# Kernel tuning notes

Measured on AMD Instinct MI355X. Metric: run time of the kernel, lower is better.

## Reference

```python
import jax, jax.numpy as jnp
import numpy as np

EPS = 1e-5

def _bn(x, s, b, m, v):
    # inference-mode BatchNorm2d over channel axis of NCHW
    return (x - m[None, :, None, None]) * jax.lax.rsqrt(v[None, :, None, None] + EPS) \
           * s[None, :, None, None] + b[None, :, None, None]

def _conv3(x, w):
    return jax.lax.conv_general_dilated(x, w, (1, 1), 'SAME',
                                        dimension_numbers=('NCHW', 'OIHW', 'NCHW'))

def _conv1(x, w, b):
    # 1x1 conv as einsum; w: [out_c, in_c]
    return jnp.einsum('oc,bchw->bohw', w, x) + b[None, :, None, None]

def _cca(f, qw, qb, kw, kb, vw, vb, gamma):
    # Criss-cross attention (faithful to source: no diagonal -inf masking, INF() unused there)
    B, C, H, W = f.shape
    q = _conv1(f, qw, qb)   # [B, C/8, H, W]
    k = _conv1(f, kw, kb)   # [B, C/8, H, W]
    v = _conv1(f, vw, vb)   # [B, C,   H, W]
    # energy along column (same w, all h') and row (same h, all w')
    eH = jnp.einsum('bchw,bciw->bhwi', q, k)            # [B,H,W,H]
    eW = jnp.einsum('bchw,bchj->bhwj', q, k)            # [B,H,W,W]
    att = jax.nn.softmax(jnp.concatenate([eH, eW], axis=3), axis=3)  # [B,H,W,H+W]
    aH, aW = att[..., :H], att[..., H:]
    oH = jnp.einsum('bhwi,bciw->bchw', aH, v)
    oW = jnp.einsum('bhwj,bchj->bchw', aW, v)
    return gamma * (oH + oW) + f


def setup_inputs() -> dict:
    key = jax.random.key(0)
    ks = iter(jax.random.split(key, 64))
    B, Cin, H, W = 8, 2048, 64, 64
    Ci, Cq, Co = 256, 32, 512
    rn = lambda s, sc=0.02: jax.random.normal(next(ks), s, jnp.float32) * sc
    ru = lambda s: jax.random.uniform(next(ks), s, jnp.float32)
    return {
        'x': jax.random.normal(next(ks), (B, Cin, H, W), jnp.float32),
        'recurrence': 2,
        'conva_w': rn((Ci, Cin, 3, 3)),
        'bn_a_s': ru((Ci,)), 'bn_a_b': rn((Ci,), 0.1), 'bn_a_m': rn((Ci,), 0.1), 'bn_a_v': ru((Ci,)),
        'q_w': rn((Cq, Ci)), 'q_b': rn((Cq,), 0.1),
        'k_w': rn((Cq, Ci)), 'k_b': rn((Cq,), 0.1),
        'v_w': rn((Ci, Ci)), 'v_b': rn((Ci,), 0.1),
        'cca_gamma': rn((1,), 1.0),
        'convb_w': rn((Ci, Ci, 3, 3)),
        'bn_b_s': ru((Ci,)), 'bn_b_b': rn((Ci,), 0.1), 'bn_b_m': rn((Ci,), 0.1), 'bn_b_v': ru((Ci,)),
        'sq_w': rn((Ci, Ci)), 'sq_b': rn((Ci,), 0.1),
        'bn_g_s': ru((Ci,)), 'bn_g_b': rn((Ci,), 0.1), 'bn_g_m': rn((Ci,), 0.1), 'bn_g_v': ru((Ci,)),
        'fc1_w': rn((Ci // 2, Ci)), 'fc1_b': rn((Ci // 2,), 0.1),
        'fc2_w': rn((Ci, Ci // 2)), 'fc2_b': rn((Ci,), 0.1),
        'bott_w': rn((Co, Cin + 2 * Ci, 3, 3)),
        'bn_t_s': ru((Co,)), 'bn_t_b': rn((Co,), 0.1), 'bn_t_m': rn((Co,), 0.1), 'bn_t_v': ru((Co,)),
    }


def reference(x, recurrence, conva_w, bn_a_s, bn_a_b, bn_a_m, bn_a_v,
              q_w, q_b, k_w, k_b, v_w, v_b, cca_gamma,
              convb_w, bn_b_s, bn_b_b, bn_b_m, bn_b_v,
              sq_w, sq_b, bn_g_s, bn_g_b, bn_g_m, bn_g_v,
              fc1_w, fc1_b, fc2_w, fc2_b,
              bott_w, bn_t_s, bn_t_b, bn_t_m, bn_t_v):
    out = _bn(_conv3(x, conva_w), bn_a_s, bn_a_b, bn_a_m, bn_a_v)
    # Global_Avg_Pooling (SE gating) on conva output
    fm = jax.nn.relu(_bn(_conv1(out, sq_w, sq_b), bn_g_s, bn_g_b, bn_g_m, bn_g_v))
    vec = fm.mean(axis=(-2, -1))                       # [B, Ci]
    h = jax.nn.relu(vec @ fc1_w.T + fc1_b)
    gate = jax.nn.sigmoid(h @ fc2_w.T + fc2_b)
    out_gap = out * gate[:, :, None, None]
    # recurrent criss-cross attention
    for _ in range(recurrence):
        out = _cca(out, q_w, q_b, k_w, k_b, v_w, v_b, cca_gamma)
    out = _bn(_conv3(out, convb_w), bn_b_s, bn_b_b, bn_b_m, bn_b_v)
    cat = jnp.concatenate([x, out, out_gap], axis=1)   # [B, Cin+2*Ci, H, W]
    return _bn(_conv3(cat, bott_w), bn_t_s, bn_t_b, bn_t_m, bn_t_v)
```

## Files before the change

kernel.cpp:

```cpp
#include <hip/hip_runtime.h>
#include <hip/hip_bf16.h>

typedef unsigned short u16;
typedef unsigned int u32;
typedef __attribute__((ext_vector_type(8))) short short8;
typedef __attribute__((ext_vector_type(8))) unsigned short u16x8;
typedef __attribute__((ext_vector_type(4))) unsigned short u16x4;
typedef __attribute__((ext_vector_type(4))) float f32x4;

#define BN_EPS 1e-5f
#define PADW 66
#define CATC 2560

__device__ __forceinline__ u16 f2b(float f) {
    __hip_bfloat16 h = __float2bfloat16(f);
    return *reinterpret_cast<u16*>(&h);
}
__device__ __forceinline__ float b2f(u16 u) {
    __hip_bfloat16 h;
    *reinterpret_cast<u16*>(&h) = u;
    return __bfloat162float(h);
}
__device__ __forceinline__ void async_copy16(void* lds, const void* g) {
    __builtin_amdgcn_global_load_lds((const __attribute__((address_space(1))) u32*)g,
                                     (__attribute__((address_space(3))) u32*)lds, 16, 0, 0);
}
__device__ __forceinline__ void fence_() { asm volatile("" ::: "memory"); }
__device__ __forceinline__ void barrier_() { fence_(); __builtin_amdgcn_s_barrier(); fence_(); }

template<int TAPS, int BN, int EPI, int CPT, int NTILES, int KSPLIT>
__global__ __launch_bounds__(512, 2)
void gemm8(const u16* __restrict__ Ag, int cstride,
           const u16* __restrict__ Bg, int ktot_full, int klen,
           const float* __restrict__ alpha, const float* __restrict__ beta,
           u16* __restrict__ outb, int ostride, int ochoff,
           float* __restrict__ outf, int nch)
{
    constexpr int WN   = BN / 4;
    constexpr int NSUB = WN / 16;
    constexpr int NQ   = NSUB / 2;
    constexpr int BLH  = BN / 128;
    constexpr int ASZ  = 256 * 128;
    constexpr int BSZ  = BN * 128;
    const int KT = klen / 64;

    extern __shared__ __align__(16) char smem[];
    char* smA = smem;
    char* smB = smem + 2 * ASZ;

    const int tid  = threadIdx.x;
    const int lane = tid & 63;
    const int wave = tid >> 6;
    const int wr = wave >> 2;
    const int wc = wave & 3;

    const int nwg = gridDim.x;
    const int wg  = blockIdx.x;
    const int swz = (wg & 7) * (nwg >> 3) + (wg >> 3);
    const int sel = swz % (NTILES * KSPLIT);
    const int m0  = (swz / (NTILES * KSPLIT)) * 256;
    const int n0  = (sel / KSPLIT) * BN;
    const int ks  = sel % KSPLIT;
    const int kstart = ks * klen;

    const int sr = tid >> 3;
    const int sc = tid & 7;
    const int scx8 = (sc ^ (sr & 7)) * 8;
    long baseAe[4];
#pragma unroll
    for (int j = 0; j < 4; ++j) {
        int p = m0 + j * 64 + sr;
        int b = p >> 12, h = (p >> 6) & 63, w = p & 63;
        long apix = (TAPS == 1) ? ((long)(b * PADW + h + 1) * PADW + (w + 1))
                                : ((long)(b * PADW + h) * PADW + w);
        baseAe[j] = apix * cstride + scx8;
    }
    long baseBe[2 * BLH];
#pragma unroll
    for (int h = 0; h < 2; ++h)
#pragma unroll
        for (int l = 0; l < BLH; ++l)
            baseBe[h * BLH + l] = (long)(n0 + h * (BN / 2) + l * 64 + sr) * ktot_full + scx8;

    auto stA = [&](int bsel, int h, long aoff) {
#pragma unroll
        for (int l = 0; l < 2; ++l) {
            const u16* g = Ag + baseAe[2 * h + l] + aoff;
            async_copy16(smA + bsel * ASZ + h * 16384 + l * 8192 + tid * 16, g);
        }
    };
    auto stB = [&](int bsel, int h, int k0) {
#pragma unroll
        for (int l = 0; l < BLH; ++l) {
            const u16* g = Bg + baseBe[h * BLH + l] + k0;
            async_copy16(smB + bsel * BSZ + h * (BSZ / 2) + l * 8192 + tid * 16, g);
        }
    };

    const int rsel  = lane & 15;
    const int cswz0 = (((lane >> 4)     ^ (lane & 7)) << 4);
    const int cswz1 = (((4 | (lane >> 4)) ^ (lane & 7)) << 4);

    f32x4 acc[8][NSUB] = {};
    short8 a[4][2], b0[NQ][2], b1[NQ][2];

    auto ldA = [&](int bsel, int mh) {
        const char* base = smA + bsel * ASZ + (wr * 128 + mh * 64 + rsel) * 128;
#pragma unroll
        for (int mi = 0; mi < 4; ++mi) {
            a[mi][0] = *(const short8*)(base + mi * 2048 + cswz0);
            a[mi][1] = *(const short8*)(base + mi * 2048 + cswz1);
        }
    };
    auto ldB = [&](int bsel, int nh, short8 (&bb)[NQ][2]) {
        const char* base = smB + bsel * BSZ + (wc * WN + nh * (WN / 2) + rsel) * 128;
#pragma unroll
        for (int nj = 0; nj < NQ; ++nj) {
            bb[nj][0] = *(const short8*)(base + nj * 2048 + cswz0);
            bb[nj][1] = *(const short8*)(base + nj * 2048 + cswz1);
        }
    };
    auto quad = [&](int MH, int NH, short8 (&bb)[NQ][2]) {
#pragma unroll
        for (int mi = 0; mi < 4; ++mi)
#pragma unroll
            for (int nj = 0; nj < NQ; ++nj)
#pragma unroll
                for (int kk = 0; kk < 2; ++kk)
                    acc[MH * 4 + mi][NH * NQ + nj] =
                        __builtin_amdgcn_mfma_f32_16x16x32_bf16(
                            a[mi][kk], bb[nj][kk], acc[MH * 4 + mi][NH * NQ + nj], 0, 0, 0);
    };

    const int tap0 = kstart / CPT;
    int c0_ = kstart - tap0 * CPT;
    int dx_ = tap0 % 3;
    long aoff_ = ((long)dx_ + (long)(tap0 / 3) * PADW) * cstride + c0_;
    auto adv = [&]() {
        c0_ += 64; aoff_ += 64;
        if (c0_ == CPT) {
            c0_ = 0; aoff_ += (long)cstride - CPT;
            if (++dx_ == 3) { dx_ = 0; aoff_ += (long)(PADW - 3) * cstride; }
        }
    };

    stA(0, 0, aoff_); stA(0, 1, aoff_); stB(0, 0, kstart); stB(0, 1, kstart);
    adv();
    stB(1, 0, kstart + 64); stB(1, 1, kstart + 64); stA(1, 0, aoff_); stA(1, 1, aoff_);
    long paoff = aoff_;
    adv();
    int skb = kstart + 128;

    if constexpr (BN == 256) asm volatile("s_waitcnt vmcnt(8)" ::: "memory");
    else                     asm volatile("s_waitcnt vmcnt(6)" ::: "memory");
    barrier_();

    for (int kt = 0; kt < KT; ++kt) {
        const int buf = kt & 1;
        ldA(buf, 0); ldB(buf, 0, b0); ldB(buf, 1, b1);
        if (kt >= 1 && kt + 1 < KT) stA(buf ^ 1, 1, paoff);
        barrier_();
        __builtin_amdgcn_s_setprio(1);
        quad(0, 0, b0); quad(0, 1, b1);
        __builtin_amdgcn_s_setprio(0);
        barrier_();
        ldA(buf, 1);
        if (kt + 2 < KT) { stB(buf, 0, skb); stB(buf, 1, skb); stA(buf, 0, aoff_); }
        barrier_();
        __builtin_amdgcn_s_setprio(1);
        quad(1, 0, b0); quad(1, 1, b1);
        __builtin_amdgcn_s_setprio(0);
        if (kt + 2 >= KT) {
            asm volatile("s_waitcnt vmcnt(0)" ::: "memory");
        } else if constexpr (BN == 256) {
            asm volatile("s_waitcnt vmcnt(6)" ::: "memory");
        } else {
            asm volatile("s_waitcnt vmcnt(4)" ::: "memory");
        }
        barrier_();
        paoff = aoff_;
        adv(); skb += 64;
    }

    const int nl = lane & 15, mq = lane >> 4;
#pragma unroll
    for (int s = 0; s < 8; ++s) {
#pragma unroll
        for (int nj = 0; nj < NSUB; ++nj) {
            int n = n0 + wc * WN + nj * 16 + nl;
            float al = (EPI == 4) ? 1.f : alpha[n];
            float be = (EPI == 4) ? 0.f : beta[n];
#pragma unroll
            for (int r = 0; r < 4; ++r) {
                int m = m0 + wr * 128 + s * 16 + mq * 4 + r;
                float v = acc[s][nj][r] * al + be;
                if (EPI == 0) {
                    int b = m >> 12, h = (m >> 6) & 63, w = m & 63;
                    long addr = ((long)(b * PADW + h + 1) * PADW + (w + 1)) * ostride + ochoff + n;
                    outb[addr] = f2b(v);
                } else if (EPI == 2) {
                    int b = m >> 12, h = (m >> 6) & 63, w = m & 63;
                    outf[((long)(b * nch + n) << 12) + (h * 64 + w)] = v;
                } else {
                    outf[(long)ks * ((long)32768 * nch) + (long)m * nch + n] = v;
                }
            }
        }
    }
}

__global__ void combine_k(const float* __restrict__ P,
                          const float* __restrict__ alpha, const float* __restrict__ beta,
                          u16* __restrict__ dst, int dstride, int choff)
{
    int t = threadIdx.x;
    int m = blockIdx.x * 4 + (t >> 6);
    int n = (t & 63) * 4;
    int b = m >> 12, h = (m >> 6) & 63, w = m & 63;
    f32x4 v0 = *(const f32x4*)&P[(long)m * 256 + n];
    f32x4 v1 = *(const f32x4*)&P[(long)32768 * 256 + (long)m * 256 + n];
    f32x4 al = *(const f32x4*)&alpha[n];
    f32x4 be = *(const f32x4*)&beta[n];
    u16x4 r;
#pragma unroll
    for (int i = 0; i < 4; ++i) r[i] = f2b((v0[i] + v1[i]) * al[i] + be[i]);
    *(u16x4*)&dst[((long)(b * PADW + h + 1) * PADW + (w + 1)) * dstride + choff + n] = r;
}

__global__ void border_k(u16* __restrict__ cat, u16* __restrict__ f0)
{
    int i = blockIdx.x;
    int b = i / 260, r = i - b * 260;
    int ph, pw;
    if (r < 66)       { ph = 0;        pw = r; }
    else if (r < 132) { ph = 65;       pw = r - 66; }
    else if (r < 196) { ph = r - 131;  pw = 0; }
    else              { ph = r - 195;  pw = 65; }
    long pix = (long)(b * PADW + ph) * PADW + pw;
    int t = threadIdx.x;
    u16x8 z = {};
    *(u16x8*)&cat[pix * CATC + t * 8] = z;
    if (t < 64) *(u16x8*)&cat[pix * CATC + 2048 + t * 8] = z;
    if (t < 32) *(u16x8*)&f0[pix * 256 + t * 8] = z;
}

template<int TAPS, int EPI>
__global__ __launch_bounds__(256, 2)
void gemm_conv(const u16* __restrict__ A, int cstride, int cpt,
               const u16* __restrict__ Bw, int ktot,
               const float* __restrict__ alpha, const float* __restrict__ beta,
               u16* __restrict__ outb, int ostride, int ochoff,
               float* __restrict__ outf, int n_total)
{
    __shared__ u16 As[128][32];
    __shared__ u16 Bs[128][32];
    __shared__ float red[128];

    const int tid  = threadIdx.x;
    const int lane = tid & 63;
    const int wave = tid >> 6;
    const int wr = wave >> 1, wc = wave & 1;
    const int m0 = blockIdx.y * 128;
    const int n0 = blockIdx.x * 128;

    long pixbase[2];
    long browk[2];
#pragma unroll
    for (int i = 0; i < 2; ++i) {
        int row = i * 64 + (tid >> 2);
        int p = m0 + row;
        int b = p >> 12, h = (p >> 6) & 63, w = p & 63;
        if (TAPS == 1) pixbase[i] = (long)(b * PADW + h + 1) * PADW + (w + 1);
        else           pixbase[i] = (long)(b * PADW + h) * PADW + w;
        browk[i] = (long)(n0 + row) * ktot;
    }
    const int chunk = (tid & 3) * 8;

    f32x4 acc[4][4] = {};

    const int steps = ktot / 32;
    int c0 = 0, dx = 0;
    long toff = 0;
    for (int s = 0; s < steps; ++s) {
        const int k0 = s * 32;
#pragma unroll
        for (int i = 0; i < 2; ++i) {
            const u16* ga = A + (pixbase[i] + ((TAPS == 1) ? 0 : toff)) * cstride + c0 + chunk;
            async_copy16((char*)(&As[0][0]) + i * 4096 + tid * 16, ga);
            const u16* gb = Bw + browk[i] + k0 + chunk;
            async_copy16((char*)(&Bs[0][0]) + i * 4096 + tid * 16, gb);
        }
        asm volatile("s_waitcnt vmcnt(0)" ::: "memory");
        __syncthreads();

        short8 af[4], bf[4];
#pragma unroll
        for (int x = 0; x < 4; ++x) {
            af[x] = *(const short8*)&As[wr * 64 + x * 16 + (lane & 15)][(lane >> 4) * 8];
            bf[x] = *(const short8*)&Bs[wc * 64 + x * 16 + (lane & 15)][(lane >> 4) * 8];
        }
#pragma unroll
        for (int mi = 0; mi < 4; ++mi)
#pragma unroll
            for (int ni = 0; ni < 4; ++ni)
                acc[mi][ni] = __builtin_amdgcn_mfma_f32_16x16x32_bf16(af[mi], bf[ni], acc[mi][ni], 0, 0, 0);
        __syncthreads();

        c0 += 32;
        if (TAPS > 1 && c0 == cpt) {
            c0 = 0; dx++; toff += 1;
            if (dx == 3) { dx = 0; toff += PADW - 3; }
        }
    }

    const int nl = lane & 15;
    const int mq = lane >> 4;

    if (EPI == 3) {
        if (tid < 128) red[tid] = 0.f;
        __syncthreads();
#pragma unroll
        for (int ni = 0; ni < 4; ++ni) {
            int ncol = wc * 64 + ni * 16 + nl;
            int n = n0 + ncol;
            float aa = alpha[n], bb = beta[n];
            float ssum = 0.f;
#pragma unroll
            for (int mi = 0; mi < 4; ++mi)
#pragma unroll
                for (int r = 0; r < 4; ++r)
                    ssum += fmaxf(acc[mi][ni][r] * aa + bb, 0.f);
            atomicAdd(&red[ncol], ssum);
        }
        __syncthreads();
        if (tid < 128) {
            int b = m0 >> 12;
            atomicAdd(&outf[b * 256 + n0 + tid], red[tid]);
        }
    } else {
#pragma unroll
        for (int mi = 0; mi < 4; ++mi) {
#pragma unroll
            for (int r = 0; r < 4; ++r) {
                int m = m0 + wr * 64 + mi * 16 + mq * 4 + r;
#pragma unroll
                for (int ni = 0; ni < 4; ++ni) {
                    int n = n0 + wc * 64 + ni * 16 + nl;
                    float v = acc[mi][ni][r] * alpha[n] + beta[n];
                    outb[(long)m * ostride + n] = f2b(v);
                }
            }
        }
    }
}

__global__ void xpad_k(const float* __restrict__ x, u16* __restrict__ cat)
{
    __shared__ float T[64][68];
    int bh = blockIdx.y;
    int b = bh >> 6, h = bh & 63;
    int c0 = blockIdx.x * 64;
    int t = threadIdx.x;
    const float* xb = x + (((long)b * 2048 + c0) * 64 + h) * 64;
#pragma unroll
    for (int i = 0; i < 4; ++i) {
        int idx = i * 256 + t;
        int c = idx >> 4, wq = (idx & 15) * 4;
        *(f32x4*)&T[c][wq] = *(const f32x4*)&xb[(long)c * 4096 + wq];
    }
    __syncthreads();
    long pbase = ((long)(b * PADW + h + 1) * PADW + 1) * CATC + c0;
#pragma unroll
    for (int j = 0; j < 2; ++j) {
        int idx = j * 256 + t;
        int w = idx >> 3, cg = (idx & 7) * 8;
        u16x8 r;
#pragma unroll
        for (int u = 0; u < 8; ++u) r[u] = f2b(T[cg + u][w]);
        *(u16x8*)&cat[pbase + (long)w * CATC + cg] = r;
    }
}

__global__ void prep_w3(const float* __restrict__ w, u16* __restrict__ o, int O, int C)
{
    int idx = blockIdx.x * 256 + threadIdx.x;
    if (idx >= O * C) return;
    int oo = idx / C, c = idx - oo * C;
    const float* s = w + (long)idx * 9;
    long base = (long)oo * 9 * C + c;
#pragma unroll
    for (int t = 0; t < 9; ++t) o[base + (long)t * C] = f2b(s[t]);
}

__global__ void prep_qkv(const float* __restrict__ qw, const float* __restrict__ kw,
                         const float* __restrict__ vw, u16* __restrict__ o)
{
    int idx = blockIdx.x * 256 + threadIdx.x;
    int n = idx >> 8, c = idx & 255;
    float v;
    if (n < 32) v = qw[n * 256 + c];
    else if (n < 64) v = kw[(n - 32) * 256 + c];
    else if (n < 320) v = vw[(n - 64) * 256 + c];
    else v = 0.f;
    o[idx] = f2b(v);
}

__global__ void prep_cast(const float* __restrict__ w, u16* __restrict__ o, int n)
{
    int i = blockIdx.x * 256 + threadIdx.x;
    if (i < n) o[i] = f2b(w[i]);
}

__global__ void prep_ab(const float* as, const float* ab, const float* am, const float* av,
                        const float* gs, const float* gb, const float* gm, const float* gv, const float* sqb,
                        const float* bs, const float* bb, const float* bm, const float* bv,
                        const float* ts, const float* tb, const float* tm, const float* tv,
                        const float* qb, const float* kb, const float* vb,
                        float* Aa, float* Ba_, float* Ag, float* Bg, float* Ab2, float* Bb2,
                        float* At, float* Bt, float* Aq, float* Bq)
{
    int i = blockIdx.x * 256 + threadIdx.x;
    if (i < 256) { float al = as[i] * rsqrtf(av[i] + BN_EPS); Aa[i] = al; Ba_[i] = ab[i] - am[i] * al; }
    else if (i < 512) { int n = i - 256; float al = gs[n] * rsqrtf(gv[n] + BN_EPS); Ag[n] = al; Bg[n] = gb[n] - gm[n] * al + sqb[n] * al; }
    else if (i < 768) { int n = i - 512; float al = bs[n] * rsqrtf(bv[n] + BN_EPS); Ab2[n] = al; Bb2[n] = bb[n] - bm[n] * al; }
    else if (i < 1280) { int n = i - 768; float al = ts[n] * rsqrtf(tv[n] + BN_EPS); At[n] = al; Bt[n] = tb[n] - tm[n] * al; }
    else if (i < 1664) { int n = i - 1280; Aq[n] = 1.f; Bq[n] = (n < 32) ? qb[n] : (n < 64) ? kb[n - 32] : (n < 320) ? vb[n - 64] : 0.f; }
}

__global__ void gate_k(const float* __restrict__ vacc, const float* __restrict__ fc1w,
                       const float* __restrict__ fc1b, const float* __restrict__ fc2w,
                       const float* __restrict__ fc2b, float* __restrict__ gate)
{
    __shared__ float v[256], hbuf[128];
    int b = blockIdx.x, t = threadIdx.x;
    v[t] = vacc[b * 256 + t] * (1.f / 4096.f);
    __syncthreads();
    if (t < 128) {
        float s = fc1b[t];
        for (int c = 0; c < 256; ++c) s += v[c] * fc1w[t * 256 + c];
        hbuf[t] = fmaxf(s, 0.f);
    }
    __syncthreads();
    float s = fc2b[t];
    for (int j = 0; j < 128; ++j) s += hbuf[j] * fc2w[t * 128 + j];
    gate[b * 256 + t] = 1.f / (1.f + __expf(-s));
}

__global__ void gap_k(const u16* __restrict__ f0, const float* __restrict__ gate, u16* __restrict__ cat)
{
    int p = blockIdx.x, t = threadIdx.x;
    int b = p >> 12, h = (p >> 6) & 63, w = p & 63;
    long ppad = (long)(b * PADW + h + 1) * PADW + (w + 1);
    float f = b2f(f0[ppad * 256 + t]);
    cat[ppad * CATC + 2304 + t] = f2b(f * gate[b * 256 + t]);
}

__global__ void gram_k(const u16* __restrict__ qkv, float* eH, float* eW)
{
    __shared__ u16 Qs[64][32];
    __shared__ u16 Ks[64][32];
    int g = blockIdx.x;
    int mode = g >> 9;
    int bx = g & 511;
    int b = bx >> 6, s = bx & 63;
    float* e = mode ? eW : eH;
    int tid = threadIdx.x, lane = tid & 63, wave = tid >> 6;
    {
        int r = tid >> 2, ch = (tid & 3) * 8;
        long pix = (mode == 0) ? ((long)(b * 64 + r) * 64 + s) : ((long)(b * 64 + s) * 64 + r);
        const u16* gp = qkv + pix * 384;
        *(u16x8*)&Qs[r][ch] = *(const u16x8*)(gp + ch);
        *(u16x8*)&Ks[r][ch] = *(const u16x8*)(gp + 32 + ch);
    }
    __syncthreads();
    f32x4 acc[4] = {};
    short8 a = *(const short8*)&Qs[wave * 16 + (lane & 15)][(lane >> 4) * 8];
#pragma unroll
    for (int ni = 0; ni < 4; ++ni) {
        short8 bb = *(const short8*)&Ks[ni * 16 + (lane & 15)][(lane >> 4) * 8];
        acc[ni] = __builtin_amdgcn_mfma_f32_16x16x32_bf16(a, bb, acc[ni], 0, 0, 0);
    }
#pragma unroll
    for (int ni = 0; ni < 4; ++ni)
#pragma unroll
        for (int r = 0; r < 4; ++r) {
            int row = wave * 16 + (lane >> 4) * 4 + r;
            int col = ni * 16 + (lane & 15);
            long pix = (mode == 0) ? ((long)(b * 64 + row) * 64 + s) : ((long)(b * 64 + s) * 64 + row);
            e[pix * 64 + col] = acc[ni][r];
        }
}

__global__ void softmax_k(const float* __restrict__ eH, const float* __restrict__ eW,
                          u16* __restrict__ aH, u16* __restrict__ aW)
{
    long row = blockIdx.x * 4 + (threadIdx.x >> 6);
    int lane = threadIdx.x & 63;
    float v0 = eH[row * 64 + lane];
    float v1 = eW[row * 64 + lane];
    float m = fmaxf(v0, v1);
#pragma unroll
    for (int off = 32; off; off >>= 1) m = fmaxf(m, __shfl_xor(m, off));
    float e0 = __expf(v0 - m), e1 = __expf(v1 - m);
    float s = e0 + e1;
#pragma unroll
    for (int off = 32; off; off >>= 1) s += __shfl_xor(s, off);
    float inv = 1.f / s;
    aH[row * 64 + lane] = f2b(e0 * inv);
    aW[row * 64 + lane] = f2b(e1 * inv);
}

__global__ __launch_bounds__(256, 2)
void oh_k(const u16* __restrict__ aH, const u16* __restrict__ qkv, float* __restrict__ oHb)
{
    __shared__ float Al[64][68];
    __shared__ u16 Vl[64][264];
    int bx = blockIdx.x;
    int b = bx >> 6, w = bx & 63;
    int t = threadIdx.x;
#pragma unroll
    for (int pass = 0; pass < 2; ++pass) {
        int r = pass * 32 + (t >> 3);
        int ch = (t & 7) * 8;
        u16x8 v = *(const u16x8*)(aH + ((long)(b * 64 + r) * 64 + w) * 64 + ch);
        f32x4 s0, s1;
#pragma unroll
        for (int u = 0; u < 4; ++u) { s0[u] = b2f(v[u]); s1[u] = b2f(v[4 + u]); }
        *(f32x4*)&Al[r][ch] = s0;
        *(f32x4*)&Al[r][ch + 4] = s1;
    }
#pragma unroll
    for (int pass = 0; pass < 8; ++pass) {
        int i = pass * 8 + (t >> 5);
        int ch = (t & 31) * 8;
        *(u16x8*)&Vl[i][ch] = *(const u16x8*)(qkv + ((long)(b * 64 + i) * 64 + w) * 384 + 64 + ch);
    }
    __syncthreads();
    int hb = (t >> 5) * 8, cb = (t & 31) * 8;
    float acc[8][8] = {};
    for (int i = 0; i < 64; ++i) {
        float av[8], vv[8];
        u16x8 v8 = *(const u16x8*)&Vl[i][cb];
#pragma unroll
        for (int u = 0; u < 8; ++u) av[u] = Al[hb + u][i];
#pragma unroll
        for (int u = 0; u < 8; ++u) vv[u] = b2f(v8[u]);
#pragma unroll
        for (int u = 0; u < 8; ++u)
#pragma unroll
            for (int x = 0; x < 8; ++x)
                acc[u][x] += av[u] * vv[x];
    }
#pragma unroll
    for (int u = 0; u < 8; ++u) {
        long base = ((long)(b * 64 + hb + u) * 64 + w) * 256 + cb;
        f32x4 s0, s1;
#pragma unroll
        for (int x = 0; x < 4; ++x) { s0[x] = acc[u][x]; s1[x] = acc[u][4 + x]; }
        *(f32x4*)&oHb[base] = s0;
        *(f32x4*)&oHb[base + 4] = s1;
    }
}

__global__ __launch_bounds__(256, 2)
void ow_k(const u16* __restrict__ aW, const u16* __restrict__ qkv, const float* __restrict__ oHb,
          const u16* __restrict__ fin, u16* __restrict__ fout, const float* __restrict__ gamma_p)
{
    __shared__ float Al[64][68];
    __shared__ u16 Vl[64][264];
    int bx = blockIdx.x;
    int b = bx >> 6, h = bx & 63;
    int t = threadIdx.x;
    float gamma = gamma_p[0];
#pragma unroll
    for (int pass = 0; pass < 2; ++pass) {
        int r = pass * 32 + (t >> 3);
        int ch = (t & 7) * 8;
        u16x8 v = *(const u16x8*)(aW + ((long)(b * 64 + h) * 64 + r) * 64 + ch);
        f32x4 s0, s1;
#pragma unroll
        for (int u = 0; u < 4; ++u) { s0[u] = b2f(v[u]); s1[u] = b2f(v[4 + u]); }
        *(f32x4*)&Al[r][ch] = s0;
        *(f32x4*)&Al[r][ch + 4] = s1;
    }
#pragma unroll
    for (int pass = 0; pass < 8; ++pass) {
        int j = pass * 8 + (t >> 5);
        int ch = (t & 31) * 8;
        *(u16x8*)&Vl[j][ch] = *(const u16x8*)(qkv + ((long)(b * 64 + h) * 64 + j) * 384 + 64 + ch);
    }
    __syncthreads();
    int wb = (t >> 5) * 8, cb = (t & 31) * 8;
    float acc[8][8] = {};
    for (int j = 0; j < 64; ++j) {
        float av[8], vv[8];
        u16x8 v8 = *(const u16x8*)&Vl[j][cb];
#pragma unroll
        for (int u = 0; u < 8; ++u) av[u] = Al[wb + u][j];
#pragma unroll
        for (int u = 0; u < 8; ++u) vv[u] = b2f(v8[u]);
#pragma unroll
        for (int u = 0; u < 8; ++u)
#pragma unroll
            for (int x = 0; x < 8; ++x)
                acc[u][x] += av[u] * vv[x];
    }
#pragma unroll
    for (int u = 0; u < 8; ++u) {
        int w = wb + u;
        long pix = ((long)(b * 64 + h) * 64 + w) * 256 + cb;
        long pp = ((long)(b * PADW + h + 1) * PADW + (w + 1)) * 256 + cb;
        u16x8 f8 = *(const u16x8*)&fin[pp];
        f32x4 o0 = *(const f32x4*)&oHb[pix];
        f32x4 o1 = *(const f32x4*)&oHb[pix + 4];
        u16x8 r8;
#pragma unroll
        for (int x = 0; x < 8; ++x) {
            float o = acc[u][x] + ((x < 4) ? o0[x] : o1[x - 4]);
            r8[x] = f2b(gamma * o + b2f(f8[x]));
        }
        *(u16x8*)&fout[pp] = r8;
    }
}

extern "C" void kernel_launch(void* const* d_in, const int* in_sizes, int n_in,
                              void* d_out, int out_size, void* d_ws, size_t ws_size,
                              hipStream_t stream)
{
    const float* x       = (const float*)d_in[0];
    const float* conva_w = (const float*)d_in[2];
    const float* bn_a_s  = (const float*)d_in[3];
    const float* bn_a_b  = (const float*)d_in[4];
    const float* bn_a_m  = (const float*)d_in[5];
    const float* bn_a_v  = (const float*)d_in[6];
    const float* q_w     = (const float*)d_in[7];
    const float* q_b     = (const float*)d_in[8];
    const float* k_w     = (const float*)d_in[9];
    const float* k_b     = (const float*)d_in[10];
    const float* v_w     = (const float*)d_in[11];
    const float* v_b     = (const float*)d_in[12];
    const float* gamma   = (const float*)d_in[13];
    const float* convb_w = (const float*)d_in[14];
    const float* bn_b_s  = (const float*)d_in[15];
    const float* bn_b_b  = (const float*)d_in[16];
    const float* bn_b_m  = (const float*)d_in[17];
    const float* bn_b_v  = (const float*)d_in[18];
    const float* sq_w    = (const float*)d_in[19];
    const float* sq_b    = (const float*)d_in[20];
    const float* bn_g_s  = (const float*)d_in[21];
    const float* bn_g_b  = (const float*)d_in[22];
    const float* bn_g_m  = (const float*)d_in[23];
    const float* bn_g_v  = (const float*)d_in[24];
    const float* fc1_w   = (const float*)d_in[25];
    const float* fc1_b   = (const float*)d_in[26];
    const float* fc2_w   = (const float*)d_in[27];
    const float* fc2_b   = (const float*)d_in[28];
    const float* bott_w  = (const float*)d_in[29];
    const float* bn_t_s  = (const float*)d_in[30];
    const float* bn_t_b  = (const float*)d_in[31];
    const float* bn_t_m  = (const float*)d_in[32];
    const float* bn_t_v  = (const float*)d_in[33];

    char* ws = (char*)d_ws;
    size_t off = 0;
    auto alloc = [&](size_t bytes) { char* p = ws + off; off += (bytes + 255) & ~(size_t)255; return p; };

    u16*   CAT  = (u16*)  alloc((size_t)8 * PADW * PADW * CATC * 2);
    u16*   F0   = (u16*)  alloc((size_t)8 * PADW * PADW * 256 * 2);
    u16*   F1   = (u16*)  alloc((size_t)8 * PADW * PADW * 256 * 2);
    size_t cca_off = off;
    u16*   QKV  = (u16*)  alloc((size_t)32768 * 384 * 2);
    float* EH   = (float*)alloc((size_t)32768 * 64 * 4);
    float* EWb  = (float*)alloc((size_t)32768 * 64 * 4);
    u16*   AH   = (u16*)  alloc((size_t)32768 * 64 * 2);
    u16*   AW   = (u16*)  alloc((size_t)32768 * 64 * 2);
    float* OHB  = (float*)alloc((size_t)32768 * 256 * 4);
    float* P    = (float*)(ws + cca_off);
    u16*   WA   = (u16*)  alloc((size_t)256 * 18432 * 2);
    u16*   WB   = (u16*)  alloc((size_t)256 * 2304 * 2);
    u16*   WT   = (u16*)  alloc((size_t)512 * 23040 * 2);
    u16*   WQKV = (u16*)  alloc((size_t)384 * 256 * 2);
    u16*   WSQ  = (u16*)  alloc((size_t)256 * 256 * 2);
    float* Aa   = (float*)alloc(256 * 4);
    float* Ba_  = (float*)alloc(256 * 4);
    float* Ag   = (float*)alloc(256 * 4);
    float* Bg   = (float*)alloc(256 * 4);
    float* Ab2  = (float*)alloc(256 * 4);
    float* Bb2  = (float*)alloc(256 * 4);
    float* At   = (float*)alloc(512 * 4);
    float* Bt   = (float*)alloc(512 * 4);
    float* Aq   = (float*)alloc(384 * 4);
    float* Bq   = (float*)alloc(384 * 4);
    float* VACC = (float*)alloc(8 * 256 * 4);
    float* GATE = (float*)alloc(8 * 256 * 4);

    hipFuncSetAttribute((const void*)gemm8<9, 256, 4, 2048, 1, 2>,
                        hipFuncAttributeMaxDynamicSharedMemorySize, 131072);
    hipFuncSetAttribute((const void*)gemm8<9, 256, 4, 256, 1, 2>,
                        hipFuncAttributeMaxDynamicSharedMemorySize, 131072);
    hipFuncSetAttribute((const void*)gemm8<9, 256, 2, 2560, 2, 1>,
                        hipFuncAttributeMaxDynamicSharedMemorySize, 131072);

    hipMemsetAsync(VACC, 0, 8 * 256 * 4, stream);

    border_k<<<8 * 260, 256, 0, stream>>>(CAT, F0);
    prep_w3<<<(256 * 2048 + 255) / 256, 256, 0, stream>>>(conva_w, WA, 256, 2048);
    prep_w3<<<(256 * 256 + 255) / 256, 256, 0, stream>>>(convb_w, WB, 256, 256);
    prep_w3<<<(512 * 2560 + 255) / 256, 256, 0, stream>>>(bott_w, WT, 512, 2560);
    prep_qkv<<<384, 256, 0, stream>>>(q_w, k_w, v_w, WQKV);
    prep_cast<<<256, 256, 0, stream>>>(sq_w, WSQ, 65536);
    prep_ab<<<7, 256, 0, stream>>>(bn_a_s, bn_a_b, bn_a_m, bn_a_v,
                                   bn_g_s, bn_g_b, bn_g_m, bn_g_v, sq_b,
                                   bn_b_s, bn_b_b, bn_b_m, bn_b_v,
                                   bn_t_s, bn_t_b, bn_t_m, bn_t_v,
                                   q_b, k_b, v_b,
                                   Aa, Ba_, Ag, Bg, Ab2, Bb2, At, Bt, Aq, Bq);
    xpad_k<<<dim3(32, 512), 256, 0, stream>>>(x, CAT);

    gemm8<9, 256, 4, 2048, 1, 2><<<256, 512, 131072, stream>>>(
        CAT, CATC, WA, 18432, 9216, Aa, Ba_, nullptr, 0, 0, P, 256);
    combine_k<<<8192, 256, 0, stream>>>(P, Aa, Ba_, F0, 256, 0);

    gemm_conv<1, 3><<<dim3(2, 256), 256, 0, stream>>>(F0, 256, 256, WSQ, 256, Ag, Bg, nullptr, 0, 0, VACC, 0);
    gate_k<<<8, 256, 0, stream>>>(VACC, fc1_w, fc1_b, fc2_w, fc2_b, GATE);
    gap_k<<<32768, 256, 0, stream>>>(F0, GATE, CAT);

    for (int rec = 0; rec < 2; ++rec) {
        u16* fin = rec ? F1 : F0;
        u16* fout = rec ? F0 : F1;
        gemm_conv<1, 1><<<dim3(3, 256), 256, 0, stream>>>(fin, 256, 256, WQKV, 256, Aq, Bq, QKV, 384, 0, nullptr, 0);
        gram_k<<<1024, 256, 0, stream>>>(QKV, EH, EWb);
        softmax_k<<<8192, 256, 0, stream>>>(EH, EWb, AH, AW);
        oh_k<<<512, 256, 0, stream>>>(AH, QKV, OHB);
        ow_k<<<512, 256, 0, stream>>>(AW, QKV, OHB, fin, fout, gamma);
    }

    gemm8<9, 256, 4, 256, 1, 2><<<256, 512, 131072, stream>>>(
        F0, 256, WB, 2304, 1152, Ab2, Bb2, nullptr, 0, 0, P, 256);
    combine_k<<<8192, 256, 0, stream>>>(P, Ab2, Bb2, CAT, CATC, 2048);

    gemm8<9, 256, 2, 2560, 2, 1><<<256, 512, 131072, stream>>>(
        CAT, CATC, WT, 23040, 23040, At, Bt, nullptr, 0, 0, (float*)d_out, 512);
}
```

Measured before the change: 1.253 ms.

## Restructure GEMM main loop to preload both A halves and drop a barrier

```diff
diff --git a/kernel.cpp b/kernel.cpp
--- a/kernel.cpp
+++ b/kernel.cpp
@@ -102,14 +102,14 @@
     const int cswz1 = (((4 | (lane >> 4)) ^ (lane & 7)) << 4);
 
     f32x4 acc[8][NSUB] = {};
-    short8 a[4][2], b0[NQ][2], b1[NQ][2];
-
-    auto ldA = [&](int bsel, int mh) {
+    short8 a0f[4][2], a1f[4][2], b0[NQ][2], b1[NQ][2];
+
+    auto ldA = [&](int bsel, int mh, short8 (&aa)[4][2]) {
         const char* base = smA + bsel * ASZ + (wr * 128 + mh * 64 + rsel) * 128;
 #pragma unroll
         for (int mi = 0; mi < 4; ++mi) {
-            a[mi][0] = *(const short8*)(base + mi * 2048 + cswz0);
-            a[mi][1] = *(const short8*)(base + mi * 2048 + cswz1);
+            aa[mi][0] = *(const short8*)(base + mi * 2048 + cswz0);
+            aa[mi][1] = *(const short8*)(base + mi * 2048 + cswz1);
         }
     };
     auto ldB = [&](int bsel, int nh, short8 (&bb)[NQ][2]) {
@@ -120,7 +120,7 @@
             bb[nj][1] = *(const short8*)(base + nj * 2048 + cswz1);
         }
     };
-    auto quad = [&](int MH, int NH, short8 (&bb)[NQ][2]) {
+    auto quad = [&](int MH, int NH, short8 (&aa)[4][2], short8 (&bb)[NQ][2]) {
 #pragma unroll
         for (int mi = 0; mi < 4; ++mi)
 #pragma unroll
@@ -129,7 +129,7 @@
                 for (int kk = 0; kk < 2; ++kk)
                     acc[MH * 4 + mi][NH * NQ + nj] =
                         __builtin_amdgcn_mfma_f32_16x16x32_bf16(
-                            a[mi][kk], bb[nj][kk], acc[MH * 4 + mi][NH * NQ + nj], 0, 0, 0);
+                            aa[mi][kk], bb[nj][kk], acc[MH * 4 + mi][NH * NQ + nj], 0, 0, 0);
     };
 
     const int tap0 = kstart / CPT;
@@ -146,39 +146,32 @@
 
     stA(0, 0, aoff_); stA(0, 1, aoff_); stB(0, 0, kstart); stB(0, 1, kstart);
     adv();
-    stB(1, 0, kstart + 64); stB(1, 1, kstart + 64); stA(1, 0, aoff_); stA(1, 1, aoff_);
-    long paoff = aoff_;
-    adv();
+    stA(1, 0, aoff_); stA(1, 1, aoff_); stB(1, 0, kstart + 64); stB(1, 1, kstart + 64);
     int skb = kstart + 128;
 
-    if constexpr (BN == 256) asm volatile("s_waitcnt vmcnt(8)" ::: "memory");
-    else                     asm volatile("s_waitcnt vmcnt(6)" ::: "memory");
+    asm volatile("s_waitcnt vmcnt(8)" ::: "memory");
     barrier_();
 
     for (int kt = 0; kt < KT; ++kt) {
         const int buf = kt & 1;
-        ldA(buf, 0); ldB(buf, 0, b0); ldB(buf, 1, b1);
-        if (kt >= 1 && kt + 1 < KT) stA(buf ^ 1, 1, paoff);
-        barrier_();
+        ldA(buf, 0, a0f); ldB(buf, 0, b0); ldB(buf, 1, b1); ldA(buf, 1, a1f);
+        if (kt >= 1 && kt + 1 < KT) { stA(buf ^ 1, 0, aoff_); stA(buf ^ 1, 1, aoff_); }
         __builtin_amdgcn_s_setprio(1);
-        quad(0, 0, b0); quad(0, 1, b1);
+        quad(0, 0, a0f, b0);
+        quad(0, 1, a0f, b1);
         __builtin_amdgcn_s_setprio(0);
         barrier_();
-        ldA(buf, 1);
-        if (kt + 2 < KT) { stB(buf, 0, skb); stB(buf, 1, skb); stA(buf, 0, aoff_); }
+        if (kt + 2 < KT) { stB(buf, 0, skb); stB(buf, 1, skb); }
+        __builtin_amdgcn_s_setprio(1);
+        quad(1, 0, a1f, b0);
+        quad(1, 1, a1f, b1);
+        __builtin_amdgcn_s_setprio(0);
+        if (kt + 2 < KT) {
+            asm volatile("s_waitcnt vmcnt(4)" ::: "memory");
+        } else {
+            asm volatile("s_waitcnt vmcnt(0)" ::: "memory");
+        }
         barrier_();
-        __builtin_amdgcn_s_setprio(1);
-        quad(1, 0, b0); quad(1, 1, b1);
-        __builtin_amdgcn_s_setprio(0);
-        if (kt + 2 >= KT) {
-            asm volatile("s_waitcnt vmcnt(0)" ::: "memory");
-        } else if constexpr (BN == 256) {
-            asm volatile("s_waitcnt vmcnt(6)" ::: "memory");
-        } else {
-            asm volatile("s_waitcnt vmcnt(4)" ::: "memory");
-        }
-        barrier_();
-        paoff = aoff_;
         adv(); skb += 64;
     }
 
```

New measurement: 1.173 ms. 6.4% less time.
